# Performance work log

Measured on AMD Instinct MI355X. Metric: run time of the kernel, lower is better.

## Reference

```python
import jax, jax.numpy as jnp
import numpy as np

B, C, H, W = 256, 3, 224, 224
IMG_SIZE = 224
BRIGHT, CONTRAST, SAT, HUE = 0.2, 0.2, 0.2, 0.05
P_JITTER, P_CROP = 0.8, 0.5
SCALE_MIN, SCALE_MAX = 0.85, 1.0


def _blend(a, b, ratio):
    # torchvision _blend with float bound 1.0
    return jnp.clip(ratio * a + (1.0 - ratio) * b, 0.0, 1.0)


def _grayscale(x):
    # x: [B,3,H,W] -> [B,H,W]
    return 0.299 * x[:, 0] + 0.587 * x[:, 1] + 0.114 * x[:, 2]


def _adjust_hue(x, hue):
    # x: [B,3,H,W], hue: [B,1,1] offset in [-0.5,0.5]
    r, g, b = x[:, 0], x[:, 1], x[:, 2]
    maxc = jnp.maximum(jnp.maximum(r, g), b)
    minc = jnp.minimum(jnp.minimum(r, g), b)
    v = maxc
    cr = maxc - minc
    eqc = cr == 0.0
    s = cr / jnp.where(eqc, 1.0, maxc)
    crd = jnp.where(eqc, 1.0, cr)
    rc = (maxc - r) / crd
    gc = (maxc - g) / crd
    bc = (maxc - b) / crd
    h = ((maxc == r) * (bc - gc)
         + ((maxc == g) & (maxc != r)) * (2.0 + rc - bc)
         + ((maxc != g) & (maxc != r)) * (4.0 + gc - rc))
    h = jnp.mod(h / 6.0 + 1.0, 1.0)
    h = jnp.mod(h + hue, 1.0)
    # hsv -> rgb
    h6 = h * 6.0
    i = jnp.floor(h6)
    f = h6 - i
    i = i.astype(jnp.int32) % 6
    p = v * (1.0 - s)
    q = v * (1.0 - s * f)
    t = v * (1.0 - s * (1.0 - f))
    m = [(i == k) for k in range(6)]
    r2 = m[0] * v + m[1] * q + m[2] * p + m[3] * p + m[4] * t + m[5] * v
    g2 = m[0] * t + m[1] * v + m[2] * v + m[3] * q + m[4] * p + m[5] * p
    b2 = m[0] * p + m[1] * p + m[2] * t + m[3] * v + m[4] * v + m[5] * q
    return jnp.stack([r2, g2, b2], axis=1)


def _crop_resize_one(im, top, left, ch, cw):
    # im: [C,H,W]; bilinear resize of crop box to IMG_SIZE x IMG_SIZE
    Hh, Ww = im.shape[1], im.shape[2]
    S = IMG_SIZE
    ys = jnp.clip(top + (jnp.arange(S) + 0.5) * ch / S - 0.5, 0.0, Hh - 1.0)
    xs = jnp.clip(left + (jnp.arange(S) + 0.5) * cw / S - 0.5, 0.0, Ww - 1.0)
    y0 = jnp.floor(ys); x0 = jnp.floor(xs)
    wy = (ys - y0)[None, :, None]  # [1,S,1]
    wx = (xs - x0)[None, None, :]  # [1,1,S]
    y0i = y0.astype(jnp.int32); y1i = jnp.minimum(y0i + 1, Hh - 1)
    x0i = x0.astype(jnp.int32); x1i = jnp.minimum(x0i + 1, Ww - 1)
    g = lambda yi, xi: im[:, yi[:, None], xi[None, :]]  # [C,S,S]
    row0 = (1.0 - wx) * g(y0i, x0i) + wx * g(y0i, x1i)
    row1 = (1.0 - wx) * g(y1i, x0i) + wx * g(y1i, x1i)
    return (1.0 - wy) * row0 + wy * row1


def _forward(img, u_jitter, u_bright, u_contrast, u_sat, u_hue, u_crop, u_scale, u_top, u_left):
    # --- color jitter (fixed op order: brightness, contrast, saturation, hue) ---
    bf = (1.0 + (2.0 * u_bright - 1.0) * BRIGHT)[:, None, None, None]
    cf = (1.0 + (2.0 * u_contrast - 1.0) * CONTRAST)[:, None, None, None]
    sf = (1.0 + (2.0 * u_sat - 1.0) * SAT)[:, None, None, None]
    hf = ((2.0 * u_hue - 1.0) * HUE)[:, None, None]
    x = _blend(img, jnp.zeros_like(img), bf)                      # brightness
    mean_gray = _grayscale(x).mean(axis=(-2, -1))[:, None, None, None]
    x = _blend(x, mean_gray, cf)                                  # contrast
    x = _blend(x, _grayscale(x)[:, None], sf)                     # saturation
    x = _adjust_hue(x, hf)                                        # hue
    x = jnp.clip(x, 0.0, 1.0)
    jitter_on = (u_jitter < P_JITTER)[:, None, None, None]
    img = jnp.where(jitter_on, x, img)
    # --- random crop + resize back to IMG_SIZE ---
    Hh, Ww = img.shape[2], img.shape[3]
    scale = SCALE_MIN + (SCALE_MAX - SCALE_MIN) * u_scale
    ch = jnp.floor(Hh * scale)
    cw = jnp.floor(Ww * scale)
    top = jnp.clip(jnp.floor(u_top * (Hh - ch + 1.0)), 0.0, Hh - ch)
    left = jnp.clip(jnp.floor(u_left * (Ww - cw + 1.0)), 0.0, Ww - cw)
    resized = jax.vmap(_crop_resize_one)(img, top, left, ch, cw)
    crop_on = (u_crop < P_CROP)[:, None, None, None]
    return jnp.where(crop_on, resized, img)


def setup_inputs() -> dict:
    key = jax.random.key(0)
    ks = jax.random.split(key, 10)
    names = ['u_jitter', 'u_bright', 'u_contrast', 'u_sat', 'u_hue',
             'u_crop', 'u_scale', 'u_top', 'u_left']
    inp = {'img': jax.random.uniform(ks[0], (B, C, H, W), dtype=jnp.float32)}
    for i, n in enumerate(names):
        inp[n] = jax.random.uniform(ks[i + 1], (B,), dtype=jnp.float32)
    return inp


def reference(img, u_jitter, u_bright, u_contrast, u_sat, u_hue, u_crop, u_scale, u_top, u_left):
    return _forward(img, u_jitter, u_bright, u_contrast, u_sat, u_hue,
                    u_crop, u_scale, u_top, u_left)
```

## Files before the change

### kernel.cpp

```cpp
#include <hip/hip_runtime.h>


static constexpr int   kB      = 256;
static constexpr int   kHW     = 224;
static constexpr int   kNPix   = kHW * kHW;
static constexpr int   kPlane  = kNPix;
static constexpr int   kPlane4 = kNPix / 4;

__device__ __forceinline__ float clamp01(float x) {
    return fminf(fmaxf(x, 0.0f), 1.0f);
}

__device__ __forceinline__ float fast_rcp(float x) {
#if __has_builtin(__builtin_amdgcn_rcpf)
    return __builtin_amdgcn_rcpf(x);
#else
    return 1.0f / x;
#endif
}

struct Px { float r, g, b; };

__device__ __forceinline__ Px jitter_px(Px p, float bf, float cf, float sf,
                                        float hf, float oc) {
    float r = clamp01(bf * p.r);
    float g = clamp01(bf * p.g);
    float b = clamp01(bf * p.b);
    r = clamp01(cf * r + oc);
    g = clamp01(cf * g + oc);
    b = clamp01(cf * b + oc);
    float gray = 0.299f * r + 0.587f * g + 0.114f * b;
    float os = (1.0f - sf) * gray;
    r = clamp01(sf * r + os);
    g = clamp01(sf * g + os);
    b = clamp01(sf * b + os);
    float maxc = fmaxf(fmaxf(r, g), b);
    float minc = fminf(fminf(r, g), b);
    float v  = maxc;
    float cr = maxc - minc;
    bool  eqc = (cr == 0.0f);
    float s   = eqc ? 0.0f : cr * fast_rcp(maxc);
    float inv = eqc ? 1.0f : fast_rcp(cr);
    float rc = (maxc - r) * inv;
    float gc = (maxc - g) * inv;
    float bc = (maxc - b) * inv;
    float h = (maxc == r) ? (bc - gc)
            : (maxc == g) ? (2.0f + rc - bc)
                          : (4.0f + gc - rc);
    h = h * 0.16666667f + 1.0f;
    h = h - floorf(h);
    h = h + hf;
    h = h - floorf(h);
    float h6 = h * 6.0f;
    float fi = floorf(h6);
    float f  = h6 - fi;
    int   i  = ((int)fi) % 6;
    float pp = v * (1.0f - s);
    float qq = v * (1.0f - s * f);
    float tt = v * (1.0f - s * (1.0f - f));
    float r2 = (i == 1) ? qq : ((i == 2) || (i == 3)) ? pp : (i == 4) ? tt : v;
    float g2 = (i == 0) ? tt : ((i == 1) || (i == 2)) ? v  : (i == 3) ? qq : pp;
    float b2 = ((i == 0) || (i == 1)) ? pp : (i == 2) ? tt : (i == 5) ? qq : v;
    Px o;
    o.r = clamp01(r2);
    o.g = clamp01(g2);
    o.b = clamp01(b2);
    return o;
}

__global__ __launch_bounds__(1024)
void gray_mean_kernel(const float* __restrict__ img,
                      const float* __restrict__ u_jitter,
                      const float* __restrict__ u_bright,
                      float* __restrict__ gray_sum)
{
    const int b = blockIdx.x;
    if (u_jitter[b] >= 0.8f) return;
    const float bf = 1.0f + (2.0f * u_bright[b] - 1.0f) * 0.2f;
    const float4* pr = (const float4*)(img + (size_t)b * 3 * kPlane);
    const float4* pg = pr + kPlane4;
    const float4* pb = pr + 2 * kPlane4;
    float acc = 0.0f;
    for (int i = threadIdx.x; i < kPlane4; i += 1024) {
        float4 r = pr[i], g = pg[i], bl = pb[i];
        acc += 0.299f * clamp01(bf * r.x) + 0.587f * clamp01(bf * g.x) + 0.114f * clamp01(bf * bl.x);
        acc += 0.299f * clamp01(bf * r.y) + 0.587f * clamp01(bf * g.y) + 0.114f * clamp01(bf * bl.y);
        acc += 0.299f * clamp01(bf * r.z) + 0.587f * clamp01(bf * g.z) + 0.114f * clamp01(bf * bl.z);
        acc += 0.299f * clamp01(bf * r.w) + 0.587f * clamp01(bf * g.w) + 0.114f * clamp01(bf * bl.w);
    }
#pragma unroll
    for (int off = 32; off > 0; off >>= 1)
        acc += __shfl_down(acc, off);
    __shared__ float red[16];
    const int lane = threadIdx.x & 63;
    const int w    = threadIdx.x >> 6;
    if (lane == 0) red[w] = acc;
    __syncthreads();
    if (threadIdx.x == 0) {
        float s = 0.0f;
#pragma unroll
        for (int k = 0; k < 16; ++k) s += red[k];
        gray_sum[b] = s;
    }
}

__global__ __launch_bounds__(256)
void aug_main_kernel(const float* __restrict__ img,
                     const float* __restrict__ u_jitter,
                     const float* __restrict__ u_bright,
                     const float* __restrict__ u_contrast,
                     const float* __restrict__ u_sat,
                     const float* __restrict__ u_hue,
                     const float* __restrict__ u_crop,
                     const float* __restrict__ u_scale,
                     const float* __restrict__ u_top,
                     const float* __restrict__ u_left,
                     const float* __restrict__ gray_sum,
                     float* __restrict__ out)
{
    const int b   = blockIdx.y;
    const int oy0 = blockIdx.x * 4;
    const int t   = threadIdx.x;

    const bool jitter_on = u_jitter[b] < 0.8f;
    const bool crop_on   = u_crop[b]   < 0.5f;

    float bf = 1.0f, cf = 1.0f, sf = 1.0f, hf = 0.0f, oc = 0.0f;
    if (jitter_on) {
        bf = 1.0f + (2.0f * u_bright[b]   - 1.0f) * 0.2f;
        cf = 1.0f + (2.0f * u_contrast[b] - 1.0f) * 0.2f;
        sf = 1.0f + (2.0f * u_sat[b]      - 1.0f) * 0.2f;
        hf = (2.0f * u_hue[b] - 1.0f) * 0.05f;
        const float mg = gray_sum[b] * (1.0f / (float)kNPix);
        oc = (1.0f - cf) * mg;
    }

    const float* base  = img + (size_t)b * 3 * kPlane;
    float*       obase = out + (size_t)b * 3 * kPlane;

    if (!crop_on) {
        if (t < 224) {
            const int f4 = oy0 * (kHW / 4) + t;
            const float4* p4 = (const float4*)base;
            float4 r4 = p4[f4];
            float4 g4 = p4[f4 + kPlane4];
            float4 b4 = p4[f4 + 2 * kPlane4];
            if (jitter_on) {
                Px a0 = jitter_px({r4.x, g4.x, b4.x}, bf, cf, sf, hf, oc);
                Px a1 = jitter_px({r4.y, g4.y, b4.y}, bf, cf, sf, hf, oc);
                Px a2 = jitter_px({r4.z, g4.z, b4.z}, bf, cf, sf, hf, oc);
                Px a3 = jitter_px({r4.w, g4.w, b4.w}, bf, cf, sf, hf, oc);
                r4 = {a0.r, a1.r, a2.r, a3.r};
                g4 = {a0.g, a1.g, a2.g, a3.g};
                b4 = {a0.b, a1.b, a2.b, a3.b};
            }
            float4* o4 = (float4*)obase;
            o4[f4]               = r4;
            o4[f4 + kPlane4]     = g4;
            o4[f4 + 2 * kPlane4] = b4;
        }
        return;
    }

    float ch, top, left;
    {
#pragma clang fp contract(off)
        float scale = 0.85f + 0.15f * u_scale[b];
        ch = floorf(224.0f * scale);
        float rem = (224.0f - ch) + 1.0f;
        top  = fminf(fmaxf(floorf(u_top[b]  * rem), 0.0f), 224.0f - ch);
        left = fminf(fmaxf(floorf(u_left[b] * rem), 0.0f), 224.0f - ch);
    }

    int ybase;
    {
#pragma clang fp contract(off)
        float fy0 = top + ((float)oy0 + 0.5f) * ch / 224.0f - 0.5f;
        fy0 = fminf(fmaxf(fy0, 0.0f), 223.0f);
        ybase = (int)floorf(fy0);
    }
    ybase = min(ybase, kHW - 5);

    __shared__ float sm[3][5 * kHW];

    for (int p = t; p < 5 * kHW; p += 256) {
        const int r   = p / kHW;
        const int col = p - r * kHW;
        const int gi  = (ybase + r) * kHW + col;
        Px q;
        q.r = base[gi];
        q.g = base[gi + kPlane];
        q.b = base[gi + 2 * kPlane];
        if (jitter_on) q = jitter_px(q, bf, cf, sf, hf, oc);
        sm[0][p] = q.r;
        sm[1][p] = q.g;
        sm[2][p] = q.b;
    }
    __syncthreads();

    for (int o = t; o < 4 * kHW; o += 256) {
        const int dy = o / kHW;
        const int ox = o - dy * kHW;
        const int oy = oy0 + dy;
        float fy, fx;
        {
#pragma clang fp contract(off)
            fy = top  + ((float)oy + 0.5f) * ch / 224.0f - 0.5f;
            fx = left + ((float)ox + 0.5f) * ch / 224.0f - 0.5f;
        }
        fy = fminf(fmaxf(fy, 0.0f), 223.0f);
        fx = fminf(fmaxf(fx, 0.0f), 223.0f);
        const float y0f = floorf(fy), x0f = floorf(fx);
        const float wy = fy - y0f,    wx = fx - x0f;
        const int y0 = (int)y0f, x0 = (int)x0f;
        const int y1 = min(y0 + 1, kHW - 1), x1 = min(x0 + 1, kHW - 1);
        const int r0 = (y0 - ybase) * kHW;
        const int r1 = (y1 - ybase) * kHW;
        const int oo = oy * kHW + ox;
#pragma unroll
        for (int c = 0; c < 3; ++c) {
            const float v00 = sm[c][r0 + x0];
            const float v01 = sm[c][r0 + x1];
            const float v10 = sm[c][r1 + x0];
            const float v11 = sm[c][r1 + x1];
            const float a0 = (1.0f - wx) * v00 + wx * v01;
            const float a1 = (1.0f - wx) * v10 + wx * v11;
            obase[c * kPlane + oo] = (1.0f - wy) * a0 + wy * a1;
        }
    }
}

extern "C" void kernel_launch(void* const* d_in, const int* in_sizes, int n_in,
                              void* d_out, int out_size, void* d_ws, size_t ws_size,
                              hipStream_t stream) {
    const float* img = (const float*)d_in[0];
    const float* uj  = (const float*)d_in[1];
    const float* ub  = (const float*)d_in[2];
    const float* uc  = (const float*)d_in[3];
    const float* us  = (const float*)d_in[4];
    const float* uh  = (const float*)d_in[5];
    const float* ucr = (const float*)d_in[6];
    const float* usc = (const float*)d_in[7];
    const float* ut  = (const float*)d_in[8];
    const float* ul  = (const float*)d_in[9];
    float* gray_sum  = (float*)d_ws;
    float* out       = (float*)d_out;

    gray_mean_kernel<<<dim3(kB), 1024, 0, stream>>>(img, uj, ub, gray_sum);

    dim3 gridB(kHW / 4, kB, 1);
    aug_main_kernel<<<gridB, 256, 0, stream>>>(img, uj, ub, uc, us, uh,
                                               ucr, usc, ut, ul, gray_sum, out);
}
```

Measured before the change: 308.2 us.

## Process 8 output rows per block with float4 staging and vectorized crop stores

Each block now covers 8 output rows instead of 4, and stages 9 source rows instead of 5. This roughly halves the redundant halo reloads and jitter recomputation in the crop path. Source rows are loaded and written to shared memory as float4, and each thread computes four adjacent output pixels so it can issue float4 global stores. The non-crop path loops over 8 rows with all 256 threads busy. In exchange the grid has fewer, larger blocks, shared memory use grows, and each thread holds more registers.

```diff
diff --git a/kernel.cpp b/kernel.cpp
--- a/kernel.cpp
+++ b/kernel.cpp
@@ -3,9 +3,12 @@
 
 static constexpr int   kB      = 256;
 static constexpr int   kHW     = 224;
+static constexpr int   kHW4    = kHW / 4;
 static constexpr int   kNPix   = kHW * kHW;
 static constexpr int   kPlane  = kNPix;
 static constexpr int   kPlane4 = kNPix / 4;
+static constexpr int   kRows   = 8;
+static constexpr int   kSrcRows = kRows + 1;
 
 __device__ __forceinline__ float clamp01(float x) {
     return fminf(fmaxf(x, 0.0f), 1.0f);
@@ -68,6 +71,18 @@
     return o;
 }
 
+__device__ __forceinline__ void jitter_quad(float4& r4, float4& g4, float4& b4,
+                                            float bf, float cf, float sf,
+                                            float hf, float oc) {
+    Px a0 = jitter_px({r4.x, g4.x, b4.x}, bf, cf, sf, hf, oc);
+    Px a1 = jitter_px({r4.y, g4.y, b4.y}, bf, cf, sf, hf, oc);
+    Px a2 = jitter_px({r4.z, g4.z, b4.z}, bf, cf, sf, hf, oc);
+    Px a3 = jitter_px({r4.w, g4.w, b4.w}, bf, cf, sf, hf, oc);
+    r4 = {a0.r, a1.r, a2.r, a3.r};
+    g4 = {a0.g, a1.g, a2.g, a3.g};
+    b4 = {a0.b, a1.b, a2.b, a3.b};
+}
+
 __global__ __launch_bounds__(1024)
 void gray_mean_kernel(const float* __restrict__ img,
                       const float* __restrict__ u_jitter,
@@ -119,7 +134,7 @@
                      float* __restrict__ out)
 {
     const int b   = blockIdx.y;
-    const int oy0 = blockIdx.x * 4;
+    const int oy0 = blockIdx.x * kRows;
     const int t   = threadIdx.x;
 
     const bool jitter_on = u_jitter[b] < 0.8f;
@@ -135,26 +150,18 @@
         oc = (1.0f - cf) * mg;
     }
 
-    const float* base  = img + (size_t)b * 3 * kPlane;
-    float*       obase = out + (size_t)b * 3 * kPlane;
+    const float*  base  = img + (size_t)b * 3 * kPlane;
+    float*        obase = out + (size_t)b * 3 * kPlane;
+    const float4* p4    = (const float4*)base;
+    float4*       o4    = (float4*)obase;
 
     if (!crop_on) {
-        if (t < 224) {
-            const int f4 = oy0 * (kHW / 4) + t;
-            const float4* p4 = (const float4*)base;
+        for (int q = t; q < kRows * kHW4; q += 256) {
+            const int f4 = oy0 * kHW4 + q;
             float4 r4 = p4[f4];
             float4 g4 = p4[f4 + kPlane4];
             float4 b4 = p4[f4 + 2 * kPlane4];
-            if (jitter_on) {
-                Px a0 = jitter_px({r4.x, g4.x, b4.x}, bf, cf, sf, hf, oc);
-                Px a1 = jitter_px({r4.y, g4.y, b4.y}, bf, cf, sf, hf, oc);
-                Px a2 = jitter_px({r4.z, g4.z, b4.z}, bf, cf, sf, hf, oc);
-                Px a3 = jitter_px({r4.w, g4.w, b4.w}, bf, cf, sf, hf, oc);
-                r4 = {a0.r, a1.r, a2.r, a3.r};
-                g4 = {a0.g, a1.g, a2.g, a3.g};
-                b4 = {a0.b, a1.b, a2.b, a3.b};
-            }
-            float4* o4 = (float4*)obase;
+            if (jitter_on) jitter_quad(r4, g4, b4, bf, cf, sf, hf, oc);
             o4[f4]               = r4;
             o4[f4 + kPlane4]     = g4;
             o4[f4 + 2 * kPlane4] = b4;
@@ -179,54 +186,71 @@
         fy0 = fminf(fmaxf(fy0, 0.0f), 223.0f);
         ybase = (int)floorf(fy0);
     }
-    ybase = min(ybase, kHW - 5);
-
-    __shared__ float sm[3][5 * kHW];
-
-    for (int p = t; p < 5 * kHW; p += 256) {
-        const int r   = p / kHW;
-        const int col = p - r * kHW;
-        const int gi  = (ybase + r) * kHW + col;
-        Px q;
-        q.r = base[gi];
-        q.g = base[gi + kPlane];
-        q.b = base[gi + 2 * kPlane];
-        if (jitter_on) q = jitter_px(q, bf, cf, sf, hf, oc);
-        sm[0][p] = q.r;
-        sm[1][p] = q.g;
-        sm[2][p] = q.b;
+    ybase = min(ybase, kHW - kSrcRows);
+
+    __shared__ float sm[3][kSrcRows * kHW];
+
+    for (int q = t; q < kSrcRows * kHW4; q += 256) {
+        const int r  = q / kHW4;
+        const int xq = q - r * kHW4;
+        const int gi = (ybase + r) * kHW4 + xq;
+        float4 r4 = p4[gi];
+        float4 g4 = p4[gi + kPlane4];
+        float4 b4 = p4[gi + 2 * kPlane4];
+        if (jitter_on) jitter_quad(r4, g4, b4, bf, cf, sf, hf, oc);
+        const int so = r * kHW + xq * 4;
+        *(float4*)&sm[0][so] = r4;
+        *(float4*)&sm[1][so] = g4;
+        *(float4*)&sm[2][so] = b4;
     }
     __syncthreads();
 
-    for (int o = t; o < 4 * kHW; o += 256) {
-        const int dy = o / kHW;
-        const int ox = o - dy * kHW;
+    for (int q = t; q < kRows * kHW4; q += 256) {
+        const int dy = q / kHW4;
+        const int xq = q - dy * kHW4;
         const int oy = oy0 + dy;
-        float fy, fx;
+        float fy;
         {
 #pragma clang fp contract(off)
-            fy = top  + ((float)oy + 0.5f) * ch / 224.0f - 0.5f;
-            fx = left + ((float)ox + 0.5f) * ch / 224.0f - 0.5f;
+            fy = top + ((float)oy + 0.5f) * ch / 224.0f - 0.5f;
         }
         fy = fminf(fmaxf(fy, 0.0f), 223.0f);
-        fx = fminf(fmaxf(fx, 0.0f), 223.0f);
-        const float y0f = floorf(fy), x0f = floorf(fx);
-        const float wy = fy - y0f,    wx = fx - x0f;
-        const int y0 = (int)y0f, x0 = (int)x0f;
-        const int y1 = min(y0 + 1, kHW - 1), x1 = min(x0 + 1, kHW - 1);
-        const int r0 = (y0 - ybase) * kHW;
-        const int r1 = (y1 - ybase) * kHW;
-        const int oo = oy * kHW + ox;
-#pragma unroll
-        for (int c = 0; c < 3; ++c) {
-            const float v00 = sm[c][r0 + x0];
-            const float v01 = sm[c][r0 + x1];
-            const float v10 = sm[c][r1 + x0];
-            const float v11 = sm[c][r1 + x1];
-            const float a0 = (1.0f - wx) * v00 + wx * v01;
-            const float a1 = (1.0f - wx) * v10 + wx * v11;
-            obase[c * kPlane + oo] = (1.0f - wy) * a0 + wy * a1;
+        const float y0f = floorf(fy);
+        const float wy  = fy - y0f;
+        const int   y0  = (int)y0f;
+        const int   y1  = min(y0 + 1, kHW - 1);
+        const int   r0  = (y0 - ybase) * kHW;
+        const int   r1  = (y1 - ybase) * kHW;
+
+        float4 res[3];
+#pragma unroll
+        for (int j = 0; j < 4; ++j) {
+            const int ox = xq * 4 + j;
+            float fx;
+            {
+#pragma clang fp contract(off)
+                fx = left + ((float)ox + 0.5f) * ch / 224.0f - 0.5f;
+            }
+            fx = fminf(fmaxf(fx, 0.0f), 223.0f);
+            const float x0f = floorf(fx);
+            const float wx  = fx - x0f;
+            const int   x0  = (int)x0f;
+            const int   x1  = min(x0 + 1, kHW - 1);
+#pragma unroll
+            for (int c = 0; c < 3; ++c) {
+                const float v00 = sm[c][r0 + x0];
+                const float v01 = sm[c][r0 + x1];
+                const float v10 = sm[c][r1 + x0];
+                const float v11 = sm[c][r1 + x1];
+                const float a0 = (1.0f - wx) * v00 + wx * v01;
+                const float a1 = (1.0f - wx) * v10 + wx * v11;
+                ((float*)&res[c])[j] = (1.0f - wy) * a0 + wy * a1;
+            }
         }
+        const int oo = oy * kHW4 + xq;
+        o4[oo]               = res[0];
+        o4[oo + kPlane4]     = res[1];
+        o4[oo + 2 * kPlane4] = res[2];
     }
 }
 
@@ -248,7 +272,7 @@
 
     gray_mean_kernel<<<dim3(kB), 1024, 0, stream>>>(img, uj, ub, gray_sum);
 
-    dim3 gridB(kHW / 4, kB, 1);
+    dim3 gridB(kHW / kRows, kB, 1);
     aug_main_kernel<<<gridB, 256, 0, stream>>>(img, uj, ub, uc, us, uh,
                                                ucr, usc, ut, ul, gray_sum, out);
 }
```

Measured after the change: 302.2 us. 2.0% less time.
